# Optimization experiments

Measured on AMD Instinct MI355X. Metric: run time of the kernel, lower is better.

Reference implementation:

```python
import jax, jax.numpy as jnp
import numpy as np

D_MODEL = 1024
NUM_HEADS = 16
MAX_LEN = 2048
HEAD_DIM = D_MODEL // NUM_HEADS
BATCH = 4
SEQ = 1024


def setup_inputs() -> dict:
    key = jax.random.key(0)
    ks = jax.random.split(key, 5)
    return {
        "query": jax.random.normal(ks[0], (BATCH, SEQ, D_MODEL), dtype=jnp.float32),
        "key": jax.random.normal(ks[1], (BATCH, SEQ, D_MODEL), dtype=jnp.float32),
        "value": jax.random.normal(ks[2], (BATCH, SEQ, D_MODEL), dtype=jnp.float32),
        "rel_k": jax.random.normal(ks[3], (MAX_LEN, HEAD_DIM), dtype=jnp.float32),
        "rel_v": jax.random.normal(ks[4], (MAX_LEN, HEAD_DIM), dtype=jnp.float32),
    }


def reference(query, key, value, rel_k, rel_v):
    B, S, D = query.shape
    H, hd = NUM_HEADS, D // NUM_HEADS
    # (B, H, S, hd)
    q = query.reshape(B, S, H, hd).transpose(0, 2, 1, 3)
    k = key.reshape(B, S, H, hd).transpose(0, 2, 1, 3)
    v = value.reshape(B, S, H, hd).transpose(0, 2, 1, 3)
    scale = 1.0 / np.sqrt(hd).astype(np.float32)
    # content scores + relative-position key bias (q . rel_k)
    scores = jnp.einsum("bhqd,bhkd->bhqk", q, k) * scale
    scores = scores + jnp.einsum("bhqd,kd->bhqk", q, rel_k[:S])
    attn = jax.nn.softmax(scores, axis=-1)  # (B, H, S, S)
    out = jnp.einsum("bhqk,bhkd->bhqd", attn, v)
    out = out + jnp.einsum("bhqk,kd->bhqd", attn, rel_v[:S])
    return out.transpose(0, 2, 1, 3).reshape(B, S, D)
```

## Files before the change

### kernel.cpp

```cpp
#include <hip/hip_runtime.h>

#define SQ 1024
#define DM 1024
#define HD 64
#define NBH 64
#define LOG2E 1.44269504f

typedef __attribute__((ext_vector_type(8))) _Float16 v8h;
typedef __attribute__((ext_vector_type(4))) float v4f;
typedef __attribute__((ext_vector_type(4))) unsigned int v4u;

typedef __attribute__((address_space(3))) void as3_void;
typedef __attribute__((address_space(1))) const void as1_cvoid;

__device__ __forceinline__ v4f mfma_f16(v8h a, v8h b, v4f c) {
  return __builtin_amdgcn_mfma_f32_16x16x32_f16(a, b, c, 0, 0, 0);
}

__device__ __forceinline__ void gload16(const _Float16* g, v8h* l) {
  __builtin_amdgcn_global_load_lds((as1_cvoid*)g, (as3_void*)l, 16, 0, 0);
}

__device__ __forceinline__ float m3(float a, float b, float c) {
  return fmaxf(fmaxf(a, b), c);
}

__global__ __launch_bounds__(256) void prep_kernel(
    const float* __restrict__ k, const float* __restrict__ v,
    const float* __restrict__ relk, const float* __restrict__ relv,
    _Float16* __restrict__ Kh, _Float16* __restrict__ Vth)
{
  __shared__ float vt[64][65];
  int blk = blockIdx.x;
  int st = blk & 15;
  int bh = blk >> 4;
  int b = bh >> 4, h = bh & 15;
  int s0 = st * 64;
  int t = (int)threadIdx.x;
  int d = t & 63, sl4 = t >> 6;
  const float scale = 0.125f;

  #pragma unroll
  for (int i = 0; i < 16; ++i) {
    int sl = sl4 + i * 4;
    int s = s0 + sl;
    size_t gidx = ((size_t)(b * SQ + s)) * DM + h * HD + d;
    float kv = (k[gidx] * scale + relk[s * HD + d]) * LOG2E;
    float vv = v[gidx] + relv[s * HD + d];
    Kh[((size_t)(bh * SQ + s)) * HD + d] = (_Float16)kv;
    vt[sl][d] = vv;
  }
  __syncthreads();
  int sl = t & 63, d4 = t >> 6;
  #pragma unroll
  for (int i = 0; i < 16; ++i) {
    int dd = d4 + i * 4;
    Vth[((size_t)(bh * HD + dd)) * SQ + s0 + sl] = (_Float16)vt[sl][dd];
  }
}

__global__ __launch_bounds__(256) void attn_kernel(
    const float* __restrict__ qf, const _Float16* __restrict__ Kh,
    const _Float16* __restrict__ Vth, float* __restrict__ out)
{
  __shared__ v8h KlG[2 * 512];
  __shared__ v8h VlG[2 * 512];

  int tid = (int)threadIdx.x;
  int lane = tid & 63, w = tid >> 6;
  int g = lane >> 4, r15 = lane & 15;
  int bid = (int)blockIdx.x;
  int wk = (bid & 7) * 128 + (bid >> 3);
  int bh = wk >> 4, qt = wk & 15;
  int b = bh >> 4, h = bh & 15;
  int q0 = qt * 64 + w * 16;

  const float* qb = qf + ((size_t)(b * SQ + q0 + r15)) * DM + h * HD;
  v4f q00 = *(const v4f*)(qb + 8 * g);
  v4f q01 = *(const v4f*)(qb + 8 * g + 4);
  v4f q10 = *(const v4f*)(qb + 32 + 8 * g);
  v4f q11 = *(const v4f*)(qb + 32 + 8 * g + 4);
  v8h aq0, aq1;
  #pragma unroll
  for (int j = 0; j < 4; ++j) {
    aq0[j] = (_Float16)q00[j];
    aq0[4 + j] = (_Float16)q01[j];
    aq1[j] = (_Float16)q10[j];
    aq1[4 + j] = (_Float16)q11[j];
  }

  const _Float16* kb = Kh + (size_t)bh * SQ * HD;
  const _Float16* vb = Vth + (size_t)bh * HD * SQ;

  size_t kOff[2], vOff[2];
  int ldsG[2];
  #pragma unroll
  for (int j = 0; j < 2; ++j) {
    int G = w * 128 + j * 64 + lane;
    int row = G >> 3, gr = G & 7;
    int fs = (row & 3) | (((row >> 3) & 1) << 2);
    int src = gr ^ fs;
    kOff[j] = (size_t)row * HD + src * 8;
    vOff[j] = (size_t)row * SQ + src * 8;
    ldsG[j] = w * 128 + j * 64;
  }

  v4f o[4];
  #pragma unroll
  for (int c = 0; c < 4; ++c) o[c] = (v4f){0.f, 0.f, 0.f, 0.f};
  float m = -3.0e38f, l = 0.f;

  int krow[4];
  #pragma unroll
  for (int c = 0; c < 4; ++c)
    krow[c] = ((c >> 1) << 5) + ((r15 >> 2) << 3) + ((c & 1) << 2) + (r15 & 3);
  int fk = (r15 & 3) | (((r15 >> 2) & 1) << 2);
  int fv = (r15 & 3) | (((r15 >> 3) & 1) << 2);

  const int NT = SQ / 64;

  #pragma unroll
  for (int j = 0; j < 2; ++j) {
    gload16(kb + kOff[j], &KlG[ldsG[j]]);
    gload16(vb + vOff[j], &VlG[ldsG[j]]);
  }
  __syncthreads();

  for (int t0 = 0; t0 < NT; ++t0) {
    const int cur = t0 & 1;
    if (t0 < NT - 1) {
      size_t kT = (size_t)(t0 + 1) * 64 * HD;
      size_t vT = (size_t)(t0 + 1) * 64;
      #pragma unroll
      for (int j = 0; j < 2; ++j) {
        gload16(kb + kT + kOff[j], &KlG[(cur ^ 1) * 512 + ldsG[j]]);
        gload16(vb + vT + vOff[j], &VlG[(cur ^ 1) * 512 + ldsG[j]]);
      }
    }

    v4f s[4];
    #pragma unroll
    for (int c = 0; c < 4; ++c) {
      v8h kf0 = KlG[cur * 512 + krow[c] * 8 + (g ^ fk)];
      v8h kf1 = KlG[cur * 512 + krow[c] * 8 + ((4 | g) ^ fk)];
      v4f z = (v4f){0.f, 0.f, 0.f, 0.f};
      z = mfma_f16(kf0, aq0, z);
      z = mfma_f16(kf1, aq1, z);
      s[c] = z;
    }

    float pa = m3(s[0][0], s[0][1], s[0][2]);
    float pb = m3(s[0][3], s[1][0], s[1][1]);
    float pc = m3(s[1][2], s[1][3], s[2][0]);
    float pd = m3(s[2][1], s[2][2], s[2][3]);
    float pe = m3(s[3][0], s[3][1], s[3][2]);
    float pm = m3(fmaxf(pa, pb), fmaxf(pc, pd), fmaxf(pe, s[3][3]));
    if (!__all(pm - m <= 8.f)) {
      float pmr = fmaxf(pm, __shfl_xor(pm, 16));
      pmr = fmaxf(pmr, __shfl_xor(pmr, 32));
      float mnew = fmaxf(m, pmr);
      float sc = __builtin_amdgcn_exp2f(m - mnew);
      m = mnew;
      l *= sc;
      #pragma unroll
      for (int c = 0; c < 4; ++c) o[c] *= sc;
    }
    float p[16];
    #pragma unroll
    for (int c = 0; c < 4; ++c)
      #pragma unroll
      for (int r = 0; r < 4; ++r) {
        float pv = __builtin_amdgcn_exp2f(s[c][r] - m);
        s[c][r] = pv;
        p[c * 4 + r] = pv;
      }
    float s0 = (p[0] + p[1]) + (p[2] + p[3]);
    float s1 = (p[4] + p[5]) + (p[6] + p[7]);
    float s2 = (p[8] + p[9]) + (p[10] + p[11]);
    float s3 = (p[12] + p[13]) + (p[14] + p[15]);
    l += (s0 + s1) + (s2 + s3);

    v4u w0, w1;
    w0[0] = __builtin_bit_cast(unsigned int, __builtin_amdgcn_cvt_pkrtz(s[0][0], s[0][1]));
    w0[1] = __builtin_bit_cast(unsigned int, __builtin_amdgcn_cvt_pkrtz(s[0][2], s[0][3]));
    w0[2] = __builtin_bit_cast(unsigned int, __builtin_amdgcn_cvt_pkrtz(s[1][0], s[1][1]));
    w0[3] = __builtin_bit_cast(unsigned int, __builtin_amdgcn_cvt_pkrtz(s[1][2], s[1][3]));
    w1[0] = __builtin_bit_cast(unsigned int, __builtin_amdgcn_cvt_pkrtz(s[2][0], s[2][1]));
    w1[1] = __builtin_bit_cast(unsigned int, __builtin_amdgcn_cvt_pkrtz(s[2][2], s[2][3]));
    w1[2] = __builtin_bit_cast(unsigned int, __builtin_amdgcn_cvt_pkrtz(s[3][0], s[3][1]));
    w1[3] = __builtin_bit_cast(unsigned int, __builtin_amdgcn_cvt_pkrtz(s[3][2], s[3][3]));
    v8h pb0 = __builtin_bit_cast(v8h, w0);
    v8h pb1 = __builtin_bit_cast(v8h, w1);

    #pragma unroll
    for (int c = 0; c < 4; ++c) {
      int rv = 16 * c + r15;
      v8h vf0 = VlG[cur * 512 + rv * 8 + (g ^ fv)];
      v8h vf1 = VlG[cur * 512 + rv * 8 + ((4 | g) ^ fv)];
      o[c] = mfma_f16(vf0, pb0, o[c]);
      o[c] = mfma_f16(vf1, pb1, o[c]);
    }

    __syncthreads();
  }

  float lr = l;
  lr += __shfl_xor(lr, 16);
  lr += __shfl_xor(lr, 32);
  float inv = 1.f / lr;
  int qrow = q0 + r15;
  #pragma unroll
  for (int c = 0; c < 4; ++c) {
    v4f res = o[c] * inv;
    *(v4f*)(&out[((size_t)(b * SQ + qrow)) * DM + h * HD + 16 * c + 4 * g]) = res;
  }
}

extern "C" void kernel_launch(void* const* d_in, const int* in_sizes, int n_in,
                              void* d_out, int out_size, void* d_ws, size_t ws_size,
                              hipStream_t stream) {
  const float* q = (const float*)d_in[0];
  const float* k = (const float*)d_in[1];
  const float* v = (const float*)d_in[2];
  const float* relk = (const float*)d_in[3];
  const float* relv = (const float*)d_in[4];

  _Float16* Kh = (_Float16*)d_ws;
  _Float16* Vth = Kh + (size_t)NBH * SQ * HD;

  prep_kernel<<<dim3(NBH * (SQ / 64)), dim3(256), 0, stream>>>(k, v, relk, relv, Kh, Vth);
  attn_kernel<<<dim3(1024), dim3(256), 0, stream>>>(q, Kh, Vth, (float*)d_out);
}
```

Before: 48.11 us.

## Use 32-key tiles with triple-buffered async LDS loads and single barrier

```diff
diff --git a/kernel.cpp b/kernel.cpp
--- a/kernel.cpp
+++ b/kernel.cpp
@@ -63,8 +63,8 @@
     const float* __restrict__ qf, const _Float16* __restrict__ Kh,
     const _Float16* __restrict__ Vth, float* __restrict__ out)
 {
-  __shared__ v8h KlG[2 * 512];
-  __shared__ v8h VlG[2 * 512];
+  __shared__ v8h KlG[3 * 256];
+  __shared__ v8h VlG[3 * 256];
 
   int tid = (int)threadIdx.x;
   int lane = tid & 63, w = tid >> 6;
@@ -92,57 +92,53 @@
   const _Float16* kb = Kh + (size_t)bh * SQ * HD;
   const _Float16* vb = Vth + (size_t)bh * HD * SQ;
 
-  size_t kOff[2], vOff[2];
-  int ldsG[2];
-  #pragma unroll
-  for (int j = 0; j < 2; ++j) {
-    int G = w * 128 + j * 64 + lane;
+  size_t kOff, vOff;
+  {
+    int G = tid;
     int row = G >> 3, gr = G & 7;
-    int fs = (row & 3) | (((row >> 3) & 1) << 2);
-    int src = gr ^ fs;
-    kOff[j] = (size_t)row * HD + src * 8;
-    vOff[j] = (size_t)row * SQ + src * 8;
-    ldsG[j] = w * 128 + j * 64;
-  }
+    int f = (row & 3) | (((row >> 3) & 1) << 2);
+    kOff = (size_t)row * HD + (size_t)((gr ^ f) * 8);
+    int vr = G >> 2, vg = G & 3;
+    vOff = (size_t)vr * SQ + (size_t)(vg * 8);
+  }
+  int ldsW = w * 64;
 
   v4f o[4];
   #pragma unroll
   for (int c = 0; c < 4; ++c) o[c] = (v4f){0.f, 0.f, 0.f, 0.f};
   float m = -3.0e38f, l = 0.f;
 
-  int krow[4];
-  #pragma unroll
-  for (int c = 0; c < 4; ++c)
-    krow[c] = ((c >> 1) << 5) + ((r15 >> 2) << 3) + ((c & 1) << 2) + (r15 & 3);
+  int krow0 = ((r15 >> 2) << 3) + (r15 & 3);
   int fk = (r15 & 3) | (((r15 >> 2) & 1) << 2);
-  int fv = (r15 & 3) | (((r15 >> 3) & 1) << 2);
-
-  const int NT = SQ / 64;
-
-  #pragma unroll
-  for (int j = 0; j < 2; ++j) {
-    gload16(kb + kOff[j], &KlG[ldsG[j]]);
-    gload16(vb + vOff[j], &VlG[ldsG[j]]);
-  }
-  __syncthreads();
-
+
+  const int NT = SQ / 32;
+
+  gload16(kb + kOff, &KlG[ldsW]);
+  gload16(vb + vOff, &VlG[ldsW]);
+  gload16(kb + (size_t)32 * HD + kOff, &KlG[256 + ldsW]);
+  gload16(vb + 32 + vOff, &VlG[256 + ldsW]);
+
+  int cur = 0;
   for (int t0 = 0; t0 < NT; ++t0) {
-    const int cur = t0 & 1;
-    if (t0 < NT - 1) {
-      size_t kT = (size_t)(t0 + 1) * 64 * HD;
-      size_t vT = (size_t)(t0 + 1) * 64;
-      #pragma unroll
-      for (int j = 0; j < 2; ++j) {
-        gload16(kb + kT + kOff[j], &KlG[(cur ^ 1) * 512 + ldsG[j]]);
-        gload16(vb + vT + vOff[j], &VlG[(cur ^ 1) * 512 + ldsG[j]]);
-      }
-    }
-
-    v4f s[4];
+    if (t0 == NT - 1) {
+      asm volatile("s_waitcnt vmcnt(0)" ::: "memory");
+    } else {
+      asm volatile("s_waitcnt vmcnt(2)" ::: "memory");
+    }
+    __builtin_amdgcn_s_barrier();
+
+    if (t0 + 2 < NT) {
+      int bs = (cur + 2 >= 3) ? cur - 1 : cur + 2;
+      gload16(kb + (size_t)(t0 + 2) * 32 * HD + kOff, &KlG[bs * 256 + ldsW]);
+      gload16(vb + (size_t)(t0 + 2) * 32 + vOff, &VlG[bs * 256 + ldsW]);
+    }
+
+    v4f s[2];
     #pragma unroll
-    for (int c = 0; c < 4; ++c) {
-      v8h kf0 = KlG[cur * 512 + krow[c] * 8 + (g ^ fk)];
-      v8h kf1 = KlG[cur * 512 + krow[c] * 8 + ((4 | g) ^ fk)];
+    for (int c = 0; c < 2; ++c) {
+      int kr = krow0 + 4 * c;
+      v8h kf0 = KlG[cur * 256 + kr * 8 + (g ^ fk)];
+      v8h kf1 = KlG[cur * 256 + kr * 8 + ((4 | g) ^ fk)];
       v4f z = (v4f){0.f, 0.f, 0.f, 0.f};
       z = mfma_f16(kf0, aq0, z);
       z = mfma_f16(kf1, aq1, z);
@@ -150,11 +146,8 @@
     }
 
     float pa = m3(s[0][0], s[0][1], s[0][2]);
-    float pb = m3(s[0][3], s[1][0], s[1][1]);
-    float pc = m3(s[1][2], s[1][3], s[2][0]);
-    float pd = m3(s[2][1], s[2][2], s[2][3]);
-    float pe = m3(s[3][0], s[3][1], s[3][2]);
-    float pm = m3(fmaxf(pa, pb), fmaxf(pc, pd), fmaxf(pe, s[3][3]));
+    float pb2 = m3(s[0][3], s[1][0], s[1][1]);
+    float pm = m3(pa, pb2, fmaxf(s[1][2], s[1][3]));
     if (!__all(pm - m <= 8.f)) {
       float pmr = fmaxf(pm, __shfl_xor(pm, 16));
       pmr = fmaxf(pmr, __shfl_xor(pmr, 32));
@@ -165,43 +158,31 @@
       #pragma unroll
       for (int c = 0; c < 4; ++c) o[c] *= sc;
     }
-    float p[16];
+    float p[8];
     #pragma unroll
-    for (int c = 0; c < 4; ++c)
+    for (int c = 0; c < 2; ++c)
       #pragma unroll
       for (int r = 0; r < 4; ++r) {
         float pv = __builtin_amdgcn_exp2f(s[c][r] - m);
         s[c][r] = pv;
         p[c * 4 + r] = pv;
       }
-    float s0 = (p[0] + p[1]) + (p[2] + p[3]);
-    float s1 = (p[4] + p[5]) + (p[6] + p[7]);
-    float s2 = (p[8] + p[9]) + (p[10] + p[11]);
-    float s3 = (p[12] + p[13]) + (p[14] + p[15]);
-    l += (s0 + s1) + (s2 + s3);
-
-    v4u w0, w1;
+    l += ((p[0] + p[1]) + (p[2] + p[3])) + ((p[4] + p[5]) + (p[6] + p[7]));
+
+    v4u w0;
     w0[0] = __builtin_bit_cast(unsigned int, __builtin_amdgcn_cvt_pkrtz(s[0][0], s[0][1]));
     w0[1] = __builtin_bit_cast(unsigned int, __builtin_amdgcn_cvt_pkrtz(s[0][2], s[0][3]));
     w0[2] = __builtin_bit_cast(unsigned int, __builtin_amdgcn_cvt_pkrtz(s[1][0], s[1][1]));
     w0[3] = __builtin_bit_cast(unsigned int, __builtin_amdgcn_cvt_pkrtz(s[1][2], s[1][3]));
-    w1[0] = __builtin_bit_cast(unsigned int, __builtin_amdgcn_cvt_pkrtz(s[2][0], s[2][1]));
-    w1[1] = __builtin_bit_cast(unsigned int, __builtin_amdgcn_cvt_pkrtz(s[2][2], s[2][3]));
-    w1[2] = __builtin_bit_cast(unsigned int, __builtin_amdgcn_cvt_pkrtz(s[3][0], s[3][1]));
-    w1[3] = __builtin_bit_cast(unsigned int, __builtin_amdgcn_cvt_pkrtz(s[3][2], s[3][3]));
-    v8h pb0 = __builtin_bit_cast(v8h, w0);
-    v8h pb1 = __builtin_bit_cast(v8h, w1);
+    v8h pb = __builtin_bit_cast(v8h, w0);
 
     #pragma unroll
     for (int c = 0; c < 4; ++c) {
-      int rv = 16 * c + r15;
-      v8h vf0 = VlG[cur * 512 + rv * 8 + (g ^ fv)];
-      v8h vf1 = VlG[cur * 512 + rv * 8 + ((4 | g) ^ fv)];
-      o[c] = mfma_f16(vf0, pb0, o[c]);
-      o[c] = mfma_f16(vf1, pb1, o[c]);
-    }
-
-    __syncthreads();
+      v8h vf = VlG[cur * 256 + (16 * c + r15) * 4 + g];
+      o[c] = mfma_f16(vf, pb, o[c]);
+    }
+
+    cur = (cur + 1 >= 3) ? 0 : cur + 1;
   }
 
   float lr = l;
```

Measured after the change: 52.41 us. 1.09x slower.
